# Optimization experiments

Measured on AMD Instinct MI355X. Metric: run time of the kernel, lower is better.

Reference implementation:

```python
import jax, jax.numpy as jnp
import numpy as np

N_MEMORY = 128
INPUT_LEN = 512
OUTPUT_LEN = 256
N_FRAMES = 65536


def setup_inputs() -> dict:
    key = jax.random.key(0)
    k1, k2, k3, k4, k5 = jax.random.split(key, 5)
    return {
        "inputs": jax.random.normal(k1, (INPUT_LEN, N_FRAMES), dtype=jnp.float32),
        "W1": jax.random.normal(k2, (2 * N_MEMORY, INPUT_LEN), dtype=jnp.float32) * 0.05,
        "B1": jax.random.normal(k3, (2 * N_MEMORY, 1), dtype=jnp.float32) * 0.05,
        "W2": jax.random.normal(k4, (OUTPUT_LEN, N_MEMORY), dtype=jnp.float32) * 0.05,
        "B2": jax.random.normal(k5, (OUTPUT_LEN, 1), dtype=jnp.float32) * 0.05,
    }


def reference(inputs, W1, B1, W2, B2):
    # h: (2M, T)
    h = jax.nn.sigmoid(jnp.matmul(W1, inputs) + B1)
    M = W1.shape[0] // 2
    left, right = h[:M], h[M:]          # each (M, T)
    prod = left * right                  # gate product, (M, T)

    # Linear recurrence: u_0 = 0; u_t = prod[:, t-1] * u_{t-1} + (1 - left[:, t-1])
    # Affine pairs for t = 1..T-1, time-major: (T-1, M)
    a = prod[:, :-1].T
    b = (1.0 - left[:, :-1]).T

    def combine(c1, c2):
        a1, b1 = c1
        a2, b2 = c2
        return a1 * a2, a2 * b1 + b2

    _, bb = jax.lax.associative_scan(combine, (a, b))
    # u_0 = 0 => u_t = bb_t; prepend the zero initial state as column 0
    z = jnp.concatenate([jnp.zeros((M, 1), dtype=inputs.dtype), bb.T], axis=1)  # (M, T)

    out = 1.0 - jax.nn.sigmoid(jnp.matmul(W2, z) + B2)  # (output_len, T)
    return out
```

## Files before the change

### kernel.cpp

```cpp
#include <hip/hip_runtime.h>

typedef unsigned short u16;
typedef short bf16x8 __attribute__((ext_vector_type(8)));
typedef float f32x4 __attribute__((ext_vector_type(4)));

#define NF 65536
#define NSC 1024
#define NMAC 16

__device__ __forceinline__ float sigm(float x){ return 1.0f/(1.0f+__expf(-x)); }

__device__ __forceinline__ u16 f2bf(float f){
  union { float f; unsigned u; } v; v.f = f;
  unsigned r = (v.u + 0x7fffu + ((v.u >> 16) & 1u)) >> 16;
  return (u16)r;
}
__device__ __forceinline__ float bfl(unsigned p){ union{unsigned u; float f;} v; v.u = p<<16;          return v.f; }
__device__ __forceinline__ float bfh(unsigned p){ union{unsigned u; float f;} v; v.u = p & 0xffff0000u; return v.f; }

__global__ __launch_bounds__(256) void k_prep(const float* __restrict__ W1, const float* __restrict__ W2,
                                              u16* __restrict__ W1f, u16* __restrict__ W2f){
  int idx = blockIdx.x*256 + threadIdx.x;
  {
    int j  = idx & 7;
    int L  = (idx >> 3) & 63;
    int ks = (idx >> 9) & 1;
    int rt = (idx >> 10) & 15;
    int ck = idx >> 14;
    int row = 16*rt + (L & 15);
    int k   = ck*64 + ks*32 + ((L >> 4) << 3) + j;
    W1f[idx] = f2bf(W1[row*512 + k]);
  }
  if (idx < 32768){
    int j  = idx & 7;
    int L  = (idx >> 3) & 63;
    int ks = (idx >> 9) & 3;
    int rt = idx >> 11;
    int row = 16*rt + (L & 15);
    int m   = ks*32 + ((L >> 4) << 3) + j;
    W2f[idx] = f2bf(W2[row*128 + m]);
  }
}

__global__ __launch_bounds__(256, 4) void k_gemm1(const float* __restrict__ x,
        const u16* __restrict__ W1f, const float* __restrict__ B1,
        unsigned* __restrict__ AB,
        float* __restrict__ Ac, float* __restrict__ Bc){
  __shared__ __align__(16) float ls[8192];
  __shared__ __align__(16) u16  xs[4096];
  const int tid = threadIdx.x;
  const int wv = tid >> 6, L = tid & 63;
  const int q = L >> 4, ln = L & 15;
  const int g = blockIdx.x;
  const int F0 = g * 64;
  const int rt0 = 2*wv;
  const bf16x8* W1f8 = (const bf16x8*)W1f;

  f32x4 acc[4][4];
  #pragma unroll
  for (int a=0;a<4;a++)
    #pragma unroll
    for (int c=0;c<4;c++) acc[a][c] = (f32x4){0.f,0.f,0.f,0.f};

  #define XSRC(ck,i) ((const float4*)(x + (size_t)((ck)*64 + 16*wv + 4*(i) + q)*NF + F0 + ln*4))
  #define LDST(buf,i) ((float4*)(ls + (buf)*4096 + (wv*4+(i))*256 + (size_t)L*4))
  float4 vst[4];
  #pragma unroll
  for (int i=0;i<4;i++) vst[i] = *XSRC(0,i);
  #pragma unroll
  for (int i=0;i<4;i++) *LDST(0,i) = vst[i];
  #pragma unroll
  for (int i=0;i<4;i++) vst[i] = *XSRC(1,i);

  for (int ck=0; ck<8; ++ck){
    bf16x8 af[2][4];
    #pragma unroll
    for (int ks=0;ks<2;ks++){
      af[ks][0] = W1f8[ck*2048 + ((rt0  )*2+ks)*64 + L];
      af[ks][1] = W1f8[ck*2048 + ((rt0+1)*2+ks)*64 + L];
      af[ks][2] = W1f8[ck*2048 + ((rt0+8)*2+ks)*64 + L];
      af[ks][3] = W1f8[ck*2048 + ((rt0+9)*2+ks)*64 + L];
    }
    __syncthreads();
    {
      const float* lsb = ls + (ck&1)*4096;
      #pragma unroll
      for (int i=0;i<2;i++){
        int s    = tid + 256*i;
        int lns  = s & 15;
        int cc   = (s >> 4) & 3;
        int qs   = (s >> 6) & 3;
        int kss  = (s >> 8) & 1;
        const float* rp = lsb + (kss*32 + qs*8)*64 + cc*16 + lns;
        unsigned u[8];
        #pragma unroll
        for (int j=0;j<8;j++) u[j] = f2bf(rp[j*64]);
        uint4 pk;
        pk.x = u[0] | (u[1]<<16); pk.y = u[2] | (u[3]<<16);
        pk.z = u[4] | (u[5]<<16); pk.w = u[6] | (u[7]<<16);
        *(uint4*)(xs + ((cc*2+kss)*64 + qs*16 + lns)*8) = pk;
      }
    }
    __syncthreads();
    if (ck < 7){
      #pragma unroll
      for (int i=0;i<4;i++) *LDST((ck+1)&1, i) = vst[i];
      if (ck < 6){
        #pragma unroll
        for (int i=0;i<4;i++) vst[i] = *XSRC(ck+2, i);
      }
    }
    #pragma unroll
    for (int ks=0; ks<2; ++ks){
      #pragma unroll
      for (int c=0;c<4;c++){
        bf16x8 bf = ((const bf16x8*)xs)[(c*2+ks)*64 + L];
        acc[0][c] = __builtin_amdgcn_mfma_f32_16x16x32_bf16(af[ks][0], bf, acc[0][c], 0,0,0);
        acc[1][c] = __builtin_amdgcn_mfma_f32_16x16x32_bf16(af[ks][1], bf, acc[1][c], 0,0,0);
        acc[2][c] = __builtin_amdgcn_mfma_f32_16x16x32_bf16(af[ks][2], bf, acc[2][c], 0,0,0);
        acc[3][c] = __builtin_amdgcn_mfma_f32_16x16x32_bf16(af[ks][3], bf, acc[3][c], 0,0,0);
      }
    }
  }
  #undef XSRC
  #undef LDST

  float bl[2][4], br[2][4], RA[2][4], RB[2][4];
  #pragma unroll
  for (int pr=0;pr<2;pr++){
    int mb = 32*wv + 16*pr + 4*q;
    #pragma unroll
    for (int r=0;r<4;r++){ bl[pr][r] = B1[mb+r]; br[pr][r] = B1[mb+128+r]; }
  }
  #pragma unroll
  for (int c=0;c<4;c++){
    int t = F0 + 16*c + ln;
    #pragma unroll
    for (int pr=0;pr<2;pr++){
      int mb = 32*wv + 16*pr + 4*q;
      f32x4 Lv = acc[pr][c], Rv = acc[pr+2][c];
      unsigned p4[4];
      float ar[4], brr[4];
      #pragma unroll
      for (int r=0;r<4;r++){
        float le = sigm(Lv[r] + bl[pr][r]);
        float ri = sigm(Rv[r] + br[pr][r]);
        unsigned pa = f2bf(le*ri), pb = f2bf(1.0f - le);
        p4[r] = pa | (pb<<16);
        ar[r] = bfl(p4[r]); brr[r] = bfh(p4[r]);
      }
      *(uint4*)(AB + (size_t)t*128 + mb) = make_uint4(p4[0],p4[1],p4[2],p4[3]);
      #pragma unroll
      for (int r=0;r<4;r++){
        float As = ar[r], Bs = brr[r];
        #pragma unroll
        for (int d=1; d<16; d<<=1){
          float Ap = __shfl_xor(As, d);
          float Bp = __shfl_xor(Bs, d);
          Bs = (ln & d) ? fmaf(As, Bp, Bs) : fmaf(Ap, Bs, Bp);
          As *= Ap;
        }
        if (c == 0){ RA[pr][r] = As; RB[pr][r] = Bs; }
        else       { RB[pr][r] = fmaf(As, RB[pr][r], Bs); RA[pr][r] *= As; }
      }
    }
  }
  if (ln == 0){
    #pragma unroll
    for (int pr=0;pr<2;pr++){
      int mb = 32*wv + 16*pr + 4*q;
      #pragma unroll
      for (int r=0;r<4;r++){
        Ac[g*128 + mb + r] = RA[pr][r];
        Bc[g*128 + mb + r] = RB[pr][r];
      }
    }
  }
}

__global__ __launch_bounds__(256) void k_scan(const float* __restrict__ Ac, const float* __restrict__ Bc,
                                              float* __restrict__ MtA, float* __restrict__ MtB){
  __shared__ float sA[2][128], sB[2][128];
  const int j = blockIdx.x;
  const int m = threadIdx.x & 127, s4 = threadIdx.x >> 7;
  const int c0 = j*64 + s4*32;
  float A = 1.f, B = 0.f;
  #pragma unroll 8
  for (int i=0;i<32;i++){
    float a = Ac[(c0+i)*128 + m], b = Bc[(c0+i)*128 + m];
    B = fmaf(a, B, b);
    A *= a;
  }
  sA[s4][m] = A; sB[s4][m] = B;
  __syncthreads();
  if (s4 == 0){
    MtA[j*128+m] = sA[1][m] * sA[0][m];
    MtB[j*128+m] = fmaf(sA[1][m], sB[0][m], sB[1][m]);
  }
}

__global__ __launch_bounds__(256, 4) void k_apply(const unsigned* __restrict__ AB,
        const float* __restrict__ Ac, const float* __restrict__ Bc,
        const float* __restrict__ MtA, const float* __restrict__ MtB,
        const u16* __restrict__ W2f, const float* __restrict__ B2,
        float* __restrict__ out){
  __shared__ __align__(16) u16 zf[8192];
  __shared__ float sA[2][128], sB[2][128];
  const int tid = threadIdx.x;
  const int g = blockIdx.x, T0 = g*64;
  const int m = tid & 127, s4 = tid >> 7;

  float vg;
  {
    const int j = g >> 6, r0 = j << 6, n = g & 63;
    int c0 = r0 + s4*32, c1 = r0 + n; if (c1 > c0+32) c1 = c0+32;
    float A = 1.f, B = 0.f;
    for (int c = c0; c < c1; ++c){
      float a = Ac[c*128 + m], b = Bc[c*128 + m];
      B = fmaf(a, B, b);
      A *= a;
    }
    sA[s4][m] = A; sB[s4][m] = B;
    float v = 0.f;
    for (int jj=0; jj<j; ++jj) v = fmaf(MtA[jj*128+m], v, MtB[jj*128+m]);
    __syncthreads();
    v = fmaf(sA[0][m], v, sB[0][m]);
    v = fmaf(sA[1][m], v, sB[1][m]);
    vg = v;
    __syncthreads();
  }

  {
    const unsigned* abp = AB + (size_t)(T0 + s4*32)*128 + m;
    unsigned abreg[32];
    #pragma unroll
    for (int i=0;i<32;i++) abreg[i] = abp[(size_t)i*128];
    float A = 1.f, Bv = 0.f;
    #pragma unroll
    for (int i=0;i<32;i++){ Bv = fmaf(bfl(abreg[i]), Bv, bfh(abreg[i])); A *= bfl(abreg[i]); }
    sA[s4][m] = A; sB[s4][m] = Bv;
    __syncthreads();
    float v = vg;
    if (s4 == 1) v = fmaf(sA[0][m], v, sB[0][m]);
    const int base_m = (m>>5)*512 + ((m>>3)&3)*128 + (m&7);
    #pragma unroll
    for (int i=0;i<32;i++){
      int t = s4*32 + i;
      zf[base_m + (t>>4)*2048 + (t&15)*8] = f2bf(v);
      v = fmaf(bfl(abreg[i]), v, bfh(abreg[i]));
    }
  }
  __syncthreads();

  const int wv = tid >> 6, L = tid & 63;
  const int q = L >> 4, ln = L & 15;
  f32x4 acc[4][4];
  #pragma unroll
  for (int a=0;a<4;a++)
    #pragma unroll
    for (int c=0;c<4;c++) acc[a][c] = (f32x4){0.f,0.f,0.f,0.f};

  #pragma unroll
  for (int ks=0; ks<4; ++ks){
    bf16x8 af[4];
    #pragma unroll
    for (int a=0;a<4;a++) af[a] = ((const bf16x8*)W2f)[((4*wv+a)*4+ks)*64 + L];
    #pragma unroll
    for (int c=0;c<4;c++){
      bf16x8 bf = ((const bf16x8*)zf)[(c*4+ks)*64 + L];
      #pragma unroll
      for (int a=0;a<4;a++)
        acc[a][c] = __builtin_amdgcn_mfma_f32_16x16x32_bf16(af[a], bf, acc[a][c], 0,0,0);
    }
  }

  #pragma unroll
  for (int a=0;a<4;a++){
    int rowb = (4*wv+a)*16 + q*4;
    float b2[4];
    #pragma unroll
    for (int r=0;r<4;r++) b2[r] = B2[rowb+r];
    #pragma unroll
    for (int r=0;r<4;r++){
      #pragma unroll
      for (int c=0;c<4;c++)
        out[(size_t)(rowb+r)*NF + T0 + 16*c + ln] = sigm(-(acc[a][c][r] + b2[r]));
    }
  }
}

extern "C" void kernel_launch(void* const* d_in, const int* in_sizes, int n_in,
                              void* d_out, int out_size, void* d_ws, size_t ws_size,
                              hipStream_t stream) {
  const float* x  = (const float*)d_in[0];
  const float* W1 = (const float*)d_in[1];
  const float* B1 = (const float*)d_in[2];
  const float* W2 = (const float*)d_in[3];
  const float* B2 = (const float*)d_in[4];
  float* out = (float*)d_out;

  u16*      W1f = (u16*)d_ws;
  u16*      W2f = W1f + 131072;
  unsigned* AB  = (unsigned*)d_ws + 81920;
  float*    Ac  = (float*)(AB + (size_t)NF*128);
  float*    Bc  = Ac + (size_t)NSC*128;
  float*    MtA = Bc + (size_t)NSC*128;
  float*    MtB = MtA + (size_t)NMAC*128;

  k_prep <<<512, 256, 0, stream>>>(W1, W2, W1f, W2f);
  k_gemm1<<<NSC, 256, 0, stream>>>(x, W1f, B1, AB, Ac, Bc);
  k_scan <<<NMAC, 256, 0, stream>>>(Ac, Bc, MtA, MtB);
  k_apply<<<NSC, 256, 0, stream>>>(AB, Ac, Bc, MtA, MtB, W2f, B2, out);
}
```

Baseline: 305.2 us.

## Use direct global-to-LDS loads, stage AB stores through LDS, remap blocks per XCD

```diff
diff --git a/kernel.cpp b/kernel.cpp
--- a/kernel.cpp
+++ b/kernel.cpp
@@ -17,6 +17,9 @@
 }
 __device__ __forceinline__ float bfl(unsigned p){ union{unsigned u; float f;} v; v.u = p<<16;          return v.f; }
 __device__ __forceinline__ float bfh(unsigned p){ union{unsigned u; float f;} v; v.u = p & 0xffff0000u; return v.f; }
+
+#define AS1(p) ((const __attribute__((address_space(1))) unsigned int*)(p))
+#define AS3(p) ((__attribute__((address_space(3))) unsigned int*)(p))
 
 __global__ __launch_bounds__(256) void k_prep(const float* __restrict__ W1, const float* __restrict__ W2,
                                               u16* __restrict__ W1f, u16* __restrict__ W2f){
@@ -51,7 +54,8 @@
   const int tid = threadIdx.x;
   const int wv = tid >> 6, L = tid & 63;
   const int q = L >> 4, ln = L & 15;
-  const int g = blockIdx.x;
+  const int hw = blockIdx.x;
+  const int g = (hw & 7)*128 + (hw >> 3);
   const int F0 = g * 64;
   const int rt0 = 2*wv;
   const bf16x8* W1f8 = (const bf16x8*)W1f;
@@ -62,17 +66,25 @@
     #pragma unroll
     for (int c=0;c<4;c++) acc[a][c] = (f32x4){0.f,0.f,0.f,0.f};
 
-  #define XSRC(ck,i) ((const float4*)(x + (size_t)((ck)*64 + 16*wv + 4*(i) + q)*NF + F0 + ln*4))
-  #define LDST(buf,i) ((float4*)(ls + (buf)*4096 + (wv*4+(i))*256 + (size_t)L*4))
-  float4 vst[4];
-  #pragma unroll
-  for (int i=0;i<4;i++) vst[i] = *XSRC(0,i);
-  #pragma unroll
-  for (int i=0;i<4;i++) *LDST(0,i) = vst[i];
-  #pragma unroll
-  for (int i=0;i<4;i++) vst[i] = *XSRC(1,i);
+  #pragma unroll
+  for (int i=0;i<4;i++){
+    int seg = wv*4 + i;
+    __builtin_amdgcn_global_load_lds(
+      AS1(x + (size_t)(seg*4 + q)*NF + F0 + ln*4),
+      AS3(ls + seg*256), 16, 0, 0);
+  }
 
   for (int ck=0; ck<8; ++ck){
+    __syncthreads();
+    if (ck < 7){
+      #pragma unroll
+      for (int i=0;i<4;i++){
+        int seg = wv*4 + i;
+        __builtin_amdgcn_global_load_lds(
+          AS1(x + (size_t)((ck+1)*64 + seg*4 + q)*NF + F0 + ln*4),
+          AS3(ls + ((ck+1)&1)*4096 + seg*256), 16, 0, 0);
+      }
+    }
     bf16x8 af[2][4];
     #pragma unroll
     for (int ks=0;ks<2;ks++){
@@ -81,7 +93,6 @@
       af[ks][2] = W1f8[ck*2048 + ((rt0+8)*2+ks)*64 + L];
       af[ks][3] = W1f8[ck*2048 + ((rt0+9)*2+ks)*64 + L];
     }
-    __syncthreads();
     {
       const float* lsb = ls + (ck&1)*4096;
       #pragma unroll
@@ -102,14 +113,6 @@
       }
     }
     __syncthreads();
-    if (ck < 7){
-      #pragma unroll
-      for (int i=0;i<4;i++) *LDST((ck+1)&1, i) = vst[i];
-      if (ck < 6){
-        #pragma unroll
-        for (int i=0;i<4;i++) vst[i] = *XSRC(ck+2, i);
-      }
-    }
     #pragma unroll
     for (int ks=0; ks<2; ++ks){
       #pragma unroll
@@ -122,9 +125,9 @@
       }
     }
   }
-  #undef XSRC
-  #undef LDST
-
+
+  __syncthreads();
+  unsigned* lsu = (unsigned*)ls;
   float bl[2][4], br[2][4], RA[2][4], RB[2][4];
   #pragma unroll
   for (int pr=0;pr<2;pr++){
@@ -134,25 +137,22 @@
   }
   #pragma unroll
   for (int c=0;c<4;c++){
-    int t = F0 + 16*c + ln;
+    int tp = 16*c + ln;
     #pragma unroll
     for (int pr=0;pr<2;pr++){
       int mb = 32*wv + 16*pr + 4*q;
       f32x4 Lv = acc[pr][c], Rv = acc[pr+2][c];
       unsigned p4[4];
-      float ar[4], brr[4];
       #pragma unroll
       for (int r=0;r<4;r++){
         float le = sigm(Lv[r] + bl[pr][r]);
         float ri = sigm(Rv[r] + br[pr][r]);
-        unsigned pa = f2bf(le*ri), pb = f2bf(1.0f - le);
-        p4[r] = pa | (pb<<16);
-        ar[r] = bfl(p4[r]); brr[r] = bfh(p4[r]);
-      }
-      *(uint4*)(AB + (size_t)t*128 + mb) = make_uint4(p4[0],p4[1],p4[2],p4[3]);
+        p4[r] = (unsigned)f2bf(le*ri) | (((unsigned)f2bf(1.0f - le))<<16);
+      }
+      *(uint4*)(&lsu[tp*128 + (mb ^ (ln<<2))]) = make_uint4(p4[0],p4[1],p4[2],p4[3]);
       #pragma unroll
       for (int r=0;r<4;r++){
-        float As = ar[r], Bs = brr[r];
+        float As = bfl(p4[r]), Bs = bfh(p4[r]);
         #pragma unroll
         for (int d=1; d<16; d<<=1){
           float Ap = __shfl_xor(As, d);
@@ -174,6 +174,18 @@
         Ac[g*128 + mb + r] = RA[pr][r];
         Bc[g*128 + mb + r] = RB[pr][r];
       }
+    }
+  }
+  __syncthreads();
+  {
+    unsigned* dst = AB + (size_t)g*8192;
+    #pragma unroll
+    for (int k2=0;k2<8;k2++){
+      int i  = tid + 256*k2;
+      int t2 = i >> 5;
+      int mm = (i & 31) << 2;
+      uint4 v = *(const uint4*)(&lsu[t2*128 + (mm ^ ((t2&15)<<2))]);
+      *(uint4*)(dst + (size_t)i*4) = v;
     }
   }
 }
@@ -207,7 +219,9 @@
   __shared__ __align__(16) u16 zf[8192];
   __shared__ float sA[2][128], sB[2][128];
   const int tid = threadIdx.x;
-  const int g = blockIdx.x, T0 = g*64;
+  const int hw = blockIdx.x;
+  const int g = (hw & 7)*128 + (hw >> 3);
+  const int T0 = g*64;
   const int m = tid & 127, s4 = tid >> 7;
 
   float vg;
```

New measurement: 277.3 us. 9.2% less time.
